# Performance work log

Hardware: AMD Instinct MI355X
Metric: run time of the kernel (lower is better)

Reference implementation:

```python
import jax, jax.numpy as jnp
import numpy as np

VOCAB = 50257
D_MODEL = 1024
PAD_IDX = 0
B, L = 4, 4096


def setup_inputs() -> dict:
    key = jax.random.key(0)
    k1, k2, k3, k4, k5 = jax.random.split(key, 5)
    input_ids = jax.random.randint(k1, (B, L), 0, VOCAB, dtype=jnp.int64 if jax.config.jax_enable_x64 else jnp.int32)
    role_mask = jax.random.randint(k2, (B, L), 0, 2, dtype=input_ids.dtype)
    emb = jax.random.normal(k3, (VOCAB, D_MODEL), dtype=jnp.float32)
    emb = emb.at[PAD_IDX].set(0.0)  # padding_idx row is zero in nn.Embedding
    # nn.Linear weight has shape (out, in); y = x @ W.T
    scale = 1.0 / np.sqrt(D_MODEL)
    W0 = jax.random.uniform(k4, (D_MODEL, D_MODEL), dtype=jnp.float32, minval=-scale, maxval=scale)
    W1 = jax.random.uniform(k5, (D_MODEL, D_MODEL), dtype=jnp.float32, minval=-scale, maxval=scale)
    return {"input_ids": input_ids, "role_mask": role_mask, "emb": emb, "W0": W0, "W1": W1}


def reference(input_ids, role_mask, emb, W0, W1):
    # Embedding lookup: (B, L, D)
    x = emb[input_ids]
    # Per-role linear transform (2-expert routing); compute both, select by mask.
    y0 = jnp.einsum('bld,ed->ble', x, W0)
    y1 = jnp.einsum('bld,ed->ble', x, W1)
    out = jnp.where((role_mask == 1)[..., None], y1, y0)
    return out
```

## Files before the change

### kernel.cpp

```cpp
#include <hip/hip_runtime.h>


#define M_TOK   16384
#define DIM     1024
#define MT_ROWS 128
#define NTILES  130
#define XROWS   (NTILES * MT_ROWS)
#define BK      64

typedef __attribute__((ext_vector_type(8))) short short8;
typedef __attribute__((ext_vector_type(4))) float f32x4;

#define OFF_PERM 256
#define OFF_WB   66816
#define OFF_X    4261120

static __device__ __forceinline__ unsigned short f2bf(float f) {
    unsigned int u = __float_as_uint(f);
    u += 0x7fffu + ((u >> 16) & 1u);
    return (unsigned short)(u >> 16);
}

__global__ void k_init(int* perm, int* cnt) {
    int i = blockIdx.x * 256 + threadIdx.x;
    if (i < 2) cnt[i] = 0;
    if (i < XROWS) perm[i] = -1;
}

__global__ void k_perm(const int* __restrict__ role, int* perm, int* cnt) {
    int t = blockIdx.x * 256 + threadIdx.x;
    int row;
    if (role[t] == 1) { int s = atomicAdd(&cnt[1], 1); row = XROWS - 1 - s; }
    else              { int s = atomicAdd(&cnt[0], 1); row = s; }
    perm[row] = t;
}

__global__ void k_gather(const int* __restrict__ ids, const int* __restrict__ perm,
                         const float* __restrict__ emb, unsigned short* __restrict__ X) {
    int row = blockIdx.x;
    int t = threadIdx.x;
    int p = perm[row];
    ushort4 v = make_ushort4(0, 0, 0, 0);
    if (p >= 0) {
        int id = ids[p];
        float4 f = *(const float4*)(emb + (size_t)id * DIM + t * 4);
        v.x = f2bf(f.x); v.y = f2bf(f.y); v.z = f2bf(f.z); v.w = f2bf(f.w);
    }
    *(ushort4*)(X + (size_t)row * DIM + t * 4) = v;
}

__global__ void k_wconv(const float* __restrict__ W0, const float* __restrict__ W1,
                        unsigned short* __restrict__ Wb) {
    int gid = blockIdx.x * 256 + threadIdx.x;
    int idx = gid * 4;
    const float* src = (idx < 1048576) ? (W0 + idx) : (W1 + (idx - 1048576));
    float4 f = *(const float4*)src;
    ushort4 v = make_ushort4(f2bf(f.x), f2bf(f.y), f2bf(f.z), f2bf(f.w));
    *(ushort4*)(Wb + idx) = v;
}

__global__ __launch_bounds__(256, 2)
void k_gemm(const unsigned short* __restrict__ Xu, const unsigned short* __restrict__ Wbu,
            const int* __restrict__ perm, const int* __restrict__ cnt,
            float* __restrict__ out) {
    __shared__ short As[MT_ROWS * BK];
    __shared__ short Bs[MT_ROWS * BK];

    int f  = blockIdx.x;
    int mt = ((f >> 6) << 3) | (f & 7);
    int nt = (f >> 3) & 7;
    if (mt >= NTILES) return;

    int n0 = cnt[0], n1 = cnt[1];
    int T0 = (n0 + 127) >> 7, T1 = (n1 + 127) >> 7;
    int e;
    if (mt < T0)                e = 0;
    else if (mt >= NTILES - T1) e = 1;
    else return;

    const short* Ag = (const short*)Xu + (size_t)mt * MT_ROWS * DIM;
    const short* Bg = (const short*)Wbu + (size_t)e * DIM * DIM + (size_t)nt * MT_ROWS * DIM;

    int tid  = threadIdx.x;
    int lane = tid & 63;
    int w    = tid >> 6;
    int wm   = w & 1, wn = w >> 1;
    int quad = lane >> 4, lq = lane & 15;

    f32x4 acc[4][4] = {};

    for (int k0 = 0; k0 < DIM; k0 += BK) {
#pragma unroll
        for (int i = 0; i < 4; ++i) {
            int q   = w * 4 + i;
            int s   = q * 64 + lane;
            int row = s >> 3;
            int kc  = (s & 7) ^ (row & 7);
            const short* ga = Ag + row * DIM + k0 + kc * 8;
            const short* gb = Bg + row * DIM + k0 + kc * 8;
            __builtin_amdgcn_global_load_lds(
                (const __attribute__((address_space(1))) unsigned int*)ga,
                (__attribute__((address_space(3))) unsigned int*)(&As[q * 512 + lane * 8]),
                16, 0, 0);
            __builtin_amdgcn_global_load_lds(
                (const __attribute__((address_space(1))) unsigned int*)gb,
                (__attribute__((address_space(3))) unsigned int*)(&Bs[q * 512 + lane * 8]),
                16, 0, 0);
        }
        __syncthreads();

#pragma unroll
        for (int s = 0; s < 2; ++s) {
            short8 av[4], bv[4];
            int s4q = s * 4 + quad;
#pragma unroll
            for (int i = 0; i < 4; ++i) {
                int ra = wm * 64 + i * 16 + lq;
                av[i] = *(const short8*)&As[(ra * 8 + (s4q ^ (ra & 7))) * 8];
                int rb = wn * 64 + i * 16 + lq;
                bv[i] = *(const short8*)&Bs[(rb * 8 + (s4q ^ (rb & 7))) * 8];
            }
#pragma unroll
            for (int i = 0; i < 4; ++i)
#pragma unroll
                for (int j = 0; j < 4; ++j)
                    acc[i][j] = __builtin_amdgcn_mfma_f32_16x16x32_bf16(
                        av[i], bv[j], acc[i][j], 0, 0, 0);
        }
        __syncthreads();
    }

    int colbase = nt * 128 + wn * 64 + lq;
#pragma unroll
    for (int i = 0; i < 4; ++i) {
#pragma unroll
        for (int r = 0; r < 4; ++r) {
            int mrow  = mt * MT_ROWS + wm * 64 + i * 16 + quad * 4 + r;
            int token = perm[mrow];
            if (token < 0) continue;
            float* o = out + (size_t)token * DIM + colbase;
#pragma unroll
            for (int j = 0; j < 4; ++j)
                o[j * 16] = acc[i][j][r];
        }
    }
}

extern "C" void kernel_launch(void* const* d_in, const int* in_sizes, int n_in,
                              void* d_out, int out_size, void* d_ws, size_t ws_size,
                              hipStream_t stream) {
    const int*   ids  = (const int*)d_in[0];
    const int*   role = (const int*)d_in[1];
    const float* emb  = (const float*)d_in[2];
    const float* W0   = (const float*)d_in[3];
    const float* W1   = (const float*)d_in[4];
    float*       out  = (float*)d_out;

    char* ws = (char*)d_ws;
    int* cnt  = (int*)ws;
    int* perm = (int*)(ws + OFF_PERM);
    unsigned short* Wb = (unsigned short*)(ws + OFF_WB);
    unsigned short* X  = (unsigned short*)(ws + OFF_X);

    k_init  <<<(XROWS + 255) / 256, 256, 0, stream>>>(perm, cnt);
    k_perm  <<<M_TOK / 256,        256, 0, stream>>>(role, perm, cnt);
    k_gather<<<XROWS,              256, 0, stream>>>(ids, perm, emb, X);
    k_wconv <<<2 * 1048576 / 1024, 256, 0, stream>>>(W0, W1, Wb);
    k_gemm  <<<1088,               256, 0, stream>>>(X, Wb, perm, cnt, out);
}
```

Baseline: 331.8 us.

## Enlarge GEMM M-tile to 256 and fuse gather with weight conversion

The GEMM M-tile grows from 128 to 256 rows. Each wave now owns 64 rows across the full 128 columns, so the accumulator doubles to 32 MFMA tiles and each B tile is reused across more rows. The embedding gather and the weight bf16 conversion are merged into one launch, padded rows are skipped instead of being zero-written, and the init kernel becomes memsets. Risks are higher register pressure at two blocks per CU and more padding waste per expert with the larger tiles.

Result: slower. 342.9 us (+3.3%).

```diff
diff --git a/kernel.cpp b/kernel.cpp
--- a/kernel.cpp
+++ b/kernel.cpp
@@ -3,10 +3,11 @@
 
 #define M_TOK   16384
 #define DIM     1024
-#define MT_ROWS 128
-#define NTILES  130
-#define XROWS   (NTILES * MT_ROWS)
+#define MT      256
+#define NTIL    65
+#define XROWS   (NTIL * MT)
 #define BK      64
+#define WBLKS   2048
 
 typedef __attribute__((ext_vector_type(8))) short short8;
 typedef __attribute__((ext_vector_type(4))) float f32x4;
@@ -21,12 +22,6 @@
     return (unsigned short)(u >> 16);
 }
 
-__global__ void k_init(int* perm, int* cnt) {
-    int i = blockIdx.x * 256 + threadIdx.x;
-    if (i < 2) cnt[i] = 0;
-    if (i < XROWS) perm[i] = -1;
-}
-
 __global__ void k_perm(const int* __restrict__ role, int* perm, int* cnt) {
     int t = blockIdx.x * 256 + threadIdx.x;
     int row;
@@ -35,112 +30,119 @@
     perm[row] = t;
 }
 
-__global__ void k_gather(const int* __restrict__ ids, const int* __restrict__ perm,
-                         const float* __restrict__ emb, unsigned short* __restrict__ X) {
-    int row = blockIdx.x;
+__global__ void k_fused(const int* __restrict__ ids, const int* __restrict__ perm,
+                        const float* __restrict__ emb,
+                        const float* __restrict__ W0, const float* __restrict__ W1,
+                        unsigned short* __restrict__ X, unsigned short* __restrict__ Wb) {
+    int b = blockIdx.x;
     int t = threadIdx.x;
-    int p = perm[row];
-    ushort4 v = make_ushort4(0, 0, 0, 0);
-    if (p >= 0) {
+    if (b < XROWS) {
+        int p = perm[b];
+        if (p < 0) return;
         int id = ids[p];
         float4 f = *(const float4*)(emb + (size_t)id * DIM + t * 4);
-        v.x = f2bf(f.x); v.y = f2bf(f.y); v.z = f2bf(f.z); v.w = f2bf(f.w);
+        ushort4 v = make_ushort4(f2bf(f.x), f2bf(f.y), f2bf(f.z), f2bf(f.w));
+        *(ushort4*)(X + (size_t)b * DIM + t * 4) = v;
+    } else {
+        int idx = ((b - XROWS) * 256 + t) * 4;
+        const float* src = (idx < 1048576) ? (W0 + idx) : (W1 + (idx - 1048576));
+        float4 f = *(const float4*)src;
+        ushort4 v = make_ushort4(f2bf(f.x), f2bf(f.y), f2bf(f.z), f2bf(f.w));
+        *(ushort4*)(Wb + idx) = v;
     }
-    *(ushort4*)(X + (size_t)row * DIM + t * 4) = v;
-}
-
-__global__ void k_wconv(const float* __restrict__ W0, const float* __restrict__ W1,
-                        unsigned short* __restrict__ Wb) {
-    int gid = blockIdx.x * 256 + threadIdx.x;
-    int idx = gid * 4;
-    const float* src = (idx < 1048576) ? (W0 + idx) : (W1 + (idx - 1048576));
-    float4 f = *(const float4*)src;
-    ushort4 v = make_ushort4(f2bf(f.x), f2bf(f.y), f2bf(f.z), f2bf(f.w));
-    *(ushort4*)(Wb + idx) = v;
 }
 
 __global__ __launch_bounds__(256, 2)
 void k_gemm(const unsigned short* __restrict__ Xu, const unsigned short* __restrict__ Wbu,
             const int* __restrict__ perm, const int* __restrict__ cnt,
             float* __restrict__ out) {
-    __shared__ short As[MT_ROWS * BK];
-    __shared__ short Bs[MT_ROWS * BK];
+    __shared__ short As[MT * BK];
+    __shared__ short Bs[128 * BK];
 
     int f  = blockIdx.x;
     int mt = ((f >> 6) << 3) | (f & 7);
     int nt = (f >> 3) & 7;
-    if (mt >= NTILES) return;
+    if (mt >= NTIL) return;
 
     int n0 = cnt[0], n1 = cnt[1];
-    int T0 = (n0 + 127) >> 7, T1 = (n1 + 127) >> 7;
+    int T0 = (n0 + 255) >> 8, T1 = (n1 + 255) >> 8;
     int e;
-    if (mt < T0)                e = 0;
-    else if (mt >= NTILES - T1) e = 1;
+    if (mt < T0)              e = 0;
+    else if (mt >= NTIL - T1) e = 1;
     else return;
 
-    const short* Ag = (const short*)Xu + (size_t)mt * MT_ROWS * DIM;
-    const short* Bg = (const short*)Wbu + (size_t)e * DIM * DIM + (size_t)nt * MT_ROWS * DIM;
+    const short* Ag = (const short*)Xu + (size_t)mt * MT * DIM;
+    const short* Bg = (const short*)Wbu + (size_t)e * DIM * DIM + (size_t)nt * 128 * DIM;
 
     int tid  = threadIdx.x;
     int lane = tid & 63;
     int w    = tid >> 6;
-    int wm   = w & 1, wn = w >> 1;
     int quad = lane >> 4, lq = lane & 15;
 
-    f32x4 acc[4][4] = {};
+    f32x4 acc[4][8] = {};
 
     for (int k0 = 0; k0 < DIM; k0 += BK) {
 #pragma unroll
-        for (int i = 0; i < 4; ++i) {
-            int q   = w * 4 + i;
-            int s   = q * 64 + lane;
+        for (int q = 0; q < 8; ++q) {
+            int s   = q * 256 + tid;
             int row = s >> 3;
             int kc  = (s & 7) ^ (row & 7);
-            const short* ga = Ag + row * DIM + k0 + kc * 8;
-            const short* gb = Bg + row * DIM + k0 + kc * 8;
             __builtin_amdgcn_global_load_lds(
-                (const __attribute__((address_space(1))) unsigned int*)ga,
-                (__attribute__((address_space(3))) unsigned int*)(&As[q * 512 + lane * 8]),
+                (const __attribute__((address_space(1))) unsigned int*)(Ag + (size_t)row * DIM + k0 + kc * 8),
+                (__attribute__((address_space(3))) unsigned int*)(&As[s * 8]),
                 16, 0, 0);
+        }
+#pragma unroll
+        for (int q = 0; q < 4; ++q) {
+            int s   = q * 256 + tid;
+            int row = s >> 3;
+            int kc  = (s & 7) ^ (row & 7);
             __builtin_amdgcn_global_load_lds(
-                (const __attribute__((address_space(1))) unsigned int*)gb,
-                (__attribute__((address_space(3))) unsigned int*)(&Bs[q * 512 + lane * 8]),
+                (const __attribute__((address_space(1))) unsigned int*)(Bg + (size_t)row * DIM + k0 + kc * 8),
+                (__attribute__((address_space(3))) unsigned int*)(&Bs[s * 8]),
                 16, 0, 0);
         }
         __syncthreads();
 
 #pragma unroll
         for (int s = 0; s < 2; ++s) {
-            short8 av[4], bv[4];
             int s4q = s * 4 + quad;
+            short8 av[4];
 #pragma unroll
             for (int i = 0; i < 4; ++i) {
-                int ra = wm * 64 + i * 16 + lq;
+                int ra = w * 64 + i * 16 + lq;
                 av[i] = *(const short8*)&As[(ra * 8 + (s4q ^ (ra & 7))) * 8];
-                int rb = wn * 64 + i * 16 + lq;
-                bv[i] = *(const short8*)&Bs[(rb * 8 + (s4q ^ (rb & 7))) * 8];
             }
 #pragma unroll
-            for (int i = 0; i < 4; ++i)
+            for (int jh = 0; jh < 2; ++jh) {
+                short8 bv[4];
 #pragma unroll
-                for (int j = 0; j < 4; ++j)
-                    acc[i][j] = __builtin_amdgcn_mfma_f32_16x16x32_bf16(
-                        av[i], bv[j], acc[i][j], 0, 0, 0);
+                for (int j = 0; j < 4; ++j) {
+                    int rb = jh * 64 + j * 16 + lq;
+                    bv[j] = *(const short8*)&Bs[(rb * 8 + (s4q ^ (rb & 7))) * 8];
+                }
+#pragma unroll
+                for (int i = 0; i < 4; ++i)
+#pragma unroll
+                    for (int j = 0; j < 4; ++j)
+                        acc[i][jh * 4 + j] = __builtin_amdgcn_mfma_f32_16x16x32_bf16(
+                            av[i], bv[j], acc[i][jh * 4 + j], 0, 0, 0);
+            }
         }
         __syncthreads();
     }
 
-    int colbase = nt * 128 + wn * 64 + lq;
+    int colbase = nt * 128 + lq;
 #pragma unroll
     for (int i = 0; i < 4; ++i) {
 #pragma unroll
         for (int r = 0; r < 4; ++r) {
-            int mrow  = mt * MT_ROWS + wm * 64 + i * 16 + quad * 4 + r;
+            int mrow  = mt * MT + w * 64 + i * 16 + quad * 4 + r;
             int token = perm[mrow];
             if (token < 0) continue;
             float* o = out + (size_t)token * DIM + colbase;
 #pragma unroll
-            for (int j = 0; j < 4; ++j)
+            for (int j = 0; j < 8; ++j)
                 o[j * 16] = acc[i][j][r];
         }
     }
@@ -162,9 +164,9 @@
     unsigned short* Wb = (unsigned short*)(ws + OFF_WB);
     unsigned short* X  = (unsigned short*)(ws + OFF_X);
 
-    k_init  <<<(XROWS + 255) / 256, 256, 0, stream>>>(perm, cnt);
-    k_perm  <<<M_TOK / 256,        256, 0, stream>>>(role, perm, cnt);
-    k_gather<<<XROWS,              256, 0, stream>>>(ids, perm, emb, X);
-    k_wconv <<<2 * 1048576 / 1024, 256, 0, stream>>>(W0, W1, Wb);
-    k_gemm  <<<1088,               256, 0, stream>>>(X, Wb, perm, cnt, out);
+    hipMemsetAsync(cnt,  0x00, 2 * sizeof(int),     stream);
+    hipMemsetAsync(perm, 0xFF, XROWS * sizeof(int), stream);
+    k_perm <<<M_TOK / 256,   256, 0, stream>>>(role, perm, cnt);
+    k_fused<<<XROWS + WBLKS, 256, 0, stream>>>(ids, perm, emb, W0, W1, X, Wb);
+    k_gemm <<<576,           256, 0, stream>>>(X, Wb, perm, cnt, out);
 }
```

## Fuse permutation and weight conversion kernels, skip padding rows, raise GEMM occupancy

Applied to the files above, without the earlier changes.

Merges the role permutation and the bf16 weight conversion into one launch, and replaces the perm init kernel with a memset of the two counters. The gather kernel now skips padding rows instead of writing zeros, and the GEMM masks its stores by row range rather than by a -1 sentinel. The GEMM launch bound is raised to 3 blocks per SM. The intent is to cut launch overhead and gather traffic. The risk is that padding rows of X stay uninitialised (their outputs are discarded), and the tighter launch bound may cause register spills.

Result: no change. 331.2 us (-0.2%).

```diff
diff --git a/kernel.cpp b/kernel.cpp
--- a/kernel.cpp
+++ b/kernel.cpp
@@ -3,10 +3,12 @@
 
 #define M_TOK   16384
 #define DIM     1024
-#define MT_ROWS 128
-#define NTILES  130
-#define XROWS   (NTILES * MT_ROWS)
+#define MT      128
+#define NTIL    130
+#define XROWS   (NTIL * MT)
 #define BK      64
+#define PBLK    64
+#define WBLKS   2048
 
 typedef __attribute__((ext_vector_type(8))) short short8;
 typedef __attribute__((ext_vector_type(4))) float f32x4;
@@ -21,65 +23,59 @@
     return (unsigned short)(u >> 16);
 }
 
-__global__ void k_init(int* perm, int* cnt) {
-    int i = blockIdx.x * 256 + threadIdx.x;
-    if (i < 2) cnt[i] = 0;
-    if (i < XROWS) perm[i] = -1;
-}
-
-__global__ void k_perm(const int* __restrict__ role, int* perm, int* cnt) {
-    int t = blockIdx.x * 256 + threadIdx.x;
-    int row;
-    if (role[t] == 1) { int s = atomicAdd(&cnt[1], 1); row = XROWS - 1 - s; }
-    else              { int s = atomicAdd(&cnt[0], 1); row = s; }
-    perm[row] = t;
+__global__ void k_pre(const int* __restrict__ role, int* perm, int* cnt,
+                      const float* __restrict__ W0, const float* __restrict__ W1,
+                      unsigned short* __restrict__ Wb) {
+    int b = blockIdx.x;
+    if (b < PBLK) {
+        int t = b * 256 + threadIdx.x;
+        int row;
+        if (role[t] == 1) { int s = atomicAdd(&cnt[1], 1); row = XROWS - 1 - s; }
+        else              { int s = atomicAdd(&cnt[0], 1); row = s; }
+        perm[row] = t;
+    } else {
+        int idx = ((b - PBLK) * 256 + threadIdx.x) * 4;
+        const float* src = (idx < 1048576) ? (W0 + idx) : (W1 + (idx - 1048576));
+        float4 f = *(const float4*)src;
+        *(ushort4*)(Wb + idx) = make_ushort4(f2bf(f.x), f2bf(f.y), f2bf(f.z), f2bf(f.w));
+    }
 }
 
 __global__ void k_gather(const int* __restrict__ ids, const int* __restrict__ perm,
-                         const float* __restrict__ emb, unsigned short* __restrict__ X) {
-    int row = blockIdx.x;
+                         const int* __restrict__ cnt, const float* __restrict__ emb,
+                         unsigned short* __restrict__ X) {
+    int b = blockIdx.x;
+    int n0 = cnt[0], n1 = cnt[1];
+    if (b >= n0 && b < XROWS - n1) return;
+    int p = perm[b];
+    int id = ids[p];
     int t = threadIdx.x;
-    int p = perm[row];
-    ushort4 v = make_ushort4(0, 0, 0, 0);
-    if (p >= 0) {
-        int id = ids[p];
-        float4 f = *(const float4*)(emb + (size_t)id * DIM + t * 4);
-        v.x = f2bf(f.x); v.y = f2bf(f.y); v.z = f2bf(f.z); v.w = f2bf(f.w);
-    }
-    *(ushort4*)(X + (size_t)row * DIM + t * 4) = v;
+    float4 f = *(const float4*)(emb + (size_t)id * DIM + t * 4);
+    *(ushort4*)(X + (size_t)b * DIM + t * 4) =
+        make_ushort4(f2bf(f.x), f2bf(f.y), f2bf(f.z), f2bf(f.w));
 }
 
-__global__ void k_wconv(const float* __restrict__ W0, const float* __restrict__ W1,
-                        unsigned short* __restrict__ Wb) {
-    int gid = blockIdx.x * 256 + threadIdx.x;
-    int idx = gid * 4;
-    const float* src = (idx < 1048576) ? (W0 + idx) : (W1 + (idx - 1048576));
-    float4 f = *(const float4*)src;
-    ushort4 v = make_ushort4(f2bf(f.x), f2bf(f.y), f2bf(f.z), f2bf(f.w));
-    *(ushort4*)(Wb + idx) = v;
-}
-
-__global__ __launch_bounds__(256, 2)
+__global__ __launch_bounds__(256, 3)
 void k_gemm(const unsigned short* __restrict__ Xu, const unsigned short* __restrict__ Wbu,
             const int* __restrict__ perm, const int* __restrict__ cnt,
             float* __restrict__ out) {
-    __shared__ short As[MT_ROWS * BK];
-    __shared__ short Bs[MT_ROWS * BK];
+    __shared__ short As[MT * BK];
+    __shared__ short Bs[MT * BK];
 
     int f  = blockIdx.x;
     int mt = ((f >> 6) << 3) | (f & 7);
     int nt = (f >> 3) & 7;
-    if (mt >= NTILES) return;
+    if (mt >= NTIL) return;
 
     int n0 = cnt[0], n1 = cnt[1];
     int T0 = (n0 + 127) >> 7, T1 = (n1 + 127) >> 7;
-    int e;
-    if (mt < T0)                e = 0;
-    else if (mt >= NTILES - T1) e = 1;
+    int e, lo, hi;
+    if (mt < T0)              { e = 0; lo = 0;            hi = n0;    }
+    else if (mt >= NTIL - T1) { e = 1; lo = XROWS - n1;   hi = XROWS; }
     else return;
 
-    const short* Ag = (const short*)Xu + (size_t)mt * MT_ROWS * DIM;
-    const short* Bg = (const short*)Wbu + (size_t)e * DIM * DIM + (size_t)nt * MT_ROWS * DIM;
+    const short* Ag = (const short*)Xu + (size_t)mt * MT * DIM;
+    const short* Bg = (const short*)Wbu + (size_t)e * DIM * DIM + (size_t)nt * MT * DIM;
 
     int tid  = threadIdx.x;
     int lane = tid & 63;
@@ -96,15 +92,13 @@
             int s   = q * 64 + lane;
             int row = s >> 3;
             int kc  = (s & 7) ^ (row & 7);
-            const short* ga = Ag + row * DIM + k0 + kc * 8;
-            const short* gb = Bg + row * DIM + k0 + kc * 8;
             __builtin_amdgcn_global_load_lds(
-                (const __attribute__((address_space(1))) unsigned int*)ga,
-                (__attribute__((address_space(3))) unsigned int*)(&As[q * 512 + lane * 8]),
+                (const __attribute__((address_space(1))) unsigned int*)(Ag + (size_t)row * DIM + k0 + kc * 8),
+                (__attribute__((address_space(3))) unsigned int*)(&As[s * 8]),
                 16, 0, 0);
             __builtin_amdgcn_global_load_lds(
-                (const __attribute__((address_space(1))) unsigned int*)gb,
-                (__attribute__((address_space(3))) unsigned int*)(&Bs[q * 512 + lane * 8]),
+                (const __attribute__((address_space(1))) unsigned int*)(Bg + (size_t)row * DIM + k0 + kc * 8),
+                (__attribute__((address_space(3))) unsigned int*)(&Bs[s * 8]),
                 16, 0, 0);
         }
         __syncthreads();
@@ -135,9 +129,9 @@
     for (int i = 0; i < 4; ++i) {
 #pragma unroll
         for (int r = 0; r < 4; ++r) {
-            int mrow  = mt * MT_ROWS + wm * 64 + i * 16 + quad * 4 + r;
+            int mrow = mt * MT + wm * 64 + i * 16 + quad * 4 + r;
+            if (mrow < lo || mrow >= hi) continue;
             int token = perm[mrow];
-            if (token < 0) continue;
             float* o = out + (size_t)token * DIM + colbase;
 #pragma unroll
             for (int j = 0; j < 4; ++j)
@@ -162,9 +156,8 @@
     unsigned short* Wb = (unsigned short*)(ws + OFF_WB);
     unsigned short* X  = (unsigned short*)(ws + OFF_X);
 
-    k_init  <<<(XROWS + 255) / 256, 256, 0, stream>>>(perm, cnt);
-    k_perm  <<<M_TOK / 256,        256, 0, stream>>>(role, perm, cnt);
-    k_gather<<<XROWS,              256, 0, stream>>>(ids, perm, emb, X);
-    k_wconv <<<2 * 1048576 / 1024, 256, 0, stream>>>(W0, W1, Wb);
-    k_gemm  <<<1088,               256, 0, stream>>>(X, Wb, perm, cnt, out);
+    hipMemsetAsync(cnt, 0x00, 2 * sizeof(int), stream);
+    k_pre   <<<PBLK + WBLKS, 256, 0, stream>>>(role, perm, cnt, W0, W1, Wb);
+    k_gather<<<XROWS,        256, 0, stream>>>(ids, perm, cnt, emb, X);
+    k_gemm  <<<1088,         256, 0, stream>>>(X, Wb, perm, cnt, out);
 }
```
